# Optimization experiments

Measured on AMD Instinct MI355X. Metric: run time of the kernel, lower is better.

## Reference

```python
import jax, jax.numpy as jnp
import numpy as np

B, S, D = 4, 2048, 768
H = 12
HD = D // H  # 64


def setup_inputs() -> dict:
    key = jax.random.key(0)
    k1, k2, k3 = jax.random.split(key, 3)
    x = jax.random.normal(k1, (B, S, D), dtype=jnp.float32)
    w_qkv = jax.random.normal(k2, (D, 3 * D), dtype=jnp.float32) * (1.0 / np.sqrt(D))
    b_qkv = jnp.zeros((3 * D,), dtype=jnp.float32)
    w_proj = jax.random.normal(k3, (D, D), dtype=jnp.float32) * (1.0 / np.sqrt(D))
    b_proj = jnp.zeros((D,), dtype=jnp.float32)
    return {"x": x, "w_qkv": w_qkv, "b_qkv": b_qkv, "w_proj": w_proj, "b_proj": b_proj}


def reference(x, w_qkv, b_qkv, w_proj, b_proj):
    b, s, d = x.shape
    qkv = x @ w_qkv + b_qkv                      # [B,S,3D]
    q, k, v = jnp.split(qkv, 3, axis=-1)
    # [B,S,D] -> [B,H,S,HD]
    q = q.reshape(b, s, H, HD).transpose(0, 2, 1, 3)
    k = k.reshape(b, s, H, HD).transpose(0, 2, 1, 3)
    v = v.reshape(b, s, H, HD).transpose(0, 2, 1, 3)
    scores = jnp.einsum("bhqd,bhkd->bhqk", q, k) / jnp.sqrt(jnp.float32(HD))
    causal = jnp.tril(jnp.ones((s, s), dtype=bool))
    scores = jnp.where(causal[None, None, :, :], scores, jnp.float32(-jnp.inf))
    attn = jax.nn.softmax(scores, axis=-1)       # dropout p=0.0 -> identity
    out = jnp.einsum("bhqk,bhkd->bhqd", attn, v)  # [B,H,S,HD]
    out = out.transpose(0, 2, 1, 3).reshape(b, s, d)
    return out @ w_proj + b_proj
```

## Files before the change

### kernel.cpp

```cpp
#include <hip/hip_runtime.h>
#include <hip/hip_bf16.h>

typedef __hip_bfloat16 bf16;
typedef __bf16 bf16x8 __attribute__((ext_vector_type(8)));
typedef float f32x4 __attribute__((ext_vector_type(4)));

#define MFMA(a, b, c) __builtin_amdgcn_mfma_f32_16x16x32_bf16(a, b, c, 0, 0, 0)
#define EXP2F(x) __builtin_exp2f(x)

constexpr int Bn = 4, Sn = 2048, Dn = 768, Hn = 12;
constexpr int N3 = 3 * Dn;
constexpr int Mrows = Bn * Sn;

constexpr size_t XB_OFF    = 0;
constexpr size_t WQKV_OFF  = 12582912;
constexpr size_t WPROJ_OFF = 16121856;
constexpr size_t Q_OFF     = 17301504;
constexpr size_t K_OFF     = 29884416;
constexpr size_t VT_OFF    = 42467328;
constexpr size_t O_OFF     = 55050240;

#define QSCALE 0.1803368801111243f

__device__ __forceinline__ void gload16(const void* g, void* l) {
  __builtin_amdgcn_global_load_lds((__attribute__((address_space(1))) void*)g,
                                   (__attribute__((address_space(3))) void*)l,
                                   16, 0, 0);
}

__device__ __forceinline__ unsigned short f2bfu(float f) {
  __hip_bfloat16 h = __float2bfloat16(f);
  return *reinterpret_cast<unsigned short*>(&h);
}

__global__ __launch_bounds__(256) void cvt_x_kernel(const float* __restrict__ in,
                                                    bf16* __restrict__ out, int n4) {
  int i = blockIdx.x * 256 + threadIdx.x;
  if (i >= n4) return;
  float4 f = reinterpret_cast<const float4*>(in)[i];
  ushort4 o;
  o.x = f2bfu(f.x); o.y = f2bfu(f.y); o.z = f2bfu(f.z); o.w = f2bfu(f.w);
  reinterpret_cast<ushort4*>(out)[i] = o;
}

__global__ __launch_bounds__(256) void transpose_cvt(const float* __restrict__ in,
                                                     bf16* __restrict__ out, int K, int N) {
  __shared__ float tile[32][33];
  int n0 = blockIdx.x * 32, k0 = blockIdx.y * 32;
  int tx = threadIdx.x & 31, ty = threadIdx.x >> 5;
  for (int r = ty; r < 32; r += 8)
    tile[r][tx] = in[(size_t)(k0 + r) * N + n0 + tx];
  __syncthreads();
  for (int r = ty; r < 32; r += 8)
    out[(size_t)(n0 + r) * K + k0 + tx] = __float2bfloat16(tile[tx][r]);
}

__global__ __launch_bounds__(256) void gemm_qkv(const bf16* __restrict__ A,
                                                const bf16* __restrict__ BT,
                                                const float* __restrict__ bias,
                                                bf16* __restrict__ Qo,
                                                bf16* __restrict__ Ko,
                                                bf16* __restrict__ Vt) {
  __shared__ __align__(16) bf16 As[2][128 * 32];
  __shared__ __align__(16) bf16 Bs[2][128 * 32];
  const int tid = threadIdx.x;
  const int m0 = blockIdx.x * 128, n0 = blockIdx.y * 128;
  const int w = tid >> 6, lane = tid & 63;
  const int wr = w >> 1, wc = w & 1;
  const int lr = lane & 15, lg = lane >> 4;

  f32x4 acc[4][4] = {};

  auto stage = [&](int k0, int sb) {
    for (int r = 0; r < 2; ++r) {
      int c = tid + r * 256;
      int row = c >> 2, ch = c & 3;
      int gch = ch ^ ((row >> 1) & 3);
      gload16(A + (size_t)(m0 + row) * Dn + k0 + gch * 8, &As[sb][c * 8]);
      gload16(BT + (size_t)(n0 + row) * Dn + k0 + gch * 8, &Bs[sb][c * 8]);
    }
  };

  stage(0, 0);
  __syncthreads();

  const int sw = (lr >> 1) & 3;
  const int aoff = (wr * 64 + lr) * 32 + ((lg ^ sw) << 3);
  const int boff = (wc * 64 + lr) * 32 + ((lg ^ sw) << 3);
  int buf = 0;

  for (int kt = 0; kt < 24; ++kt) {
    if (kt < 23) stage((kt + 1) * 32, buf ^ 1);
    bf16x8 af[4], bfr[4];
    for (int mi = 0; mi < 4; ++mi)
      af[mi] = *reinterpret_cast<const bf16x8*>(&As[buf][aoff + mi * 512]);
    for (int ni = 0; ni < 4; ++ni)
      bfr[ni] = *reinterpret_cast<const bf16x8*>(&Bs[buf][boff + ni * 512]);
    for (int mi = 0; mi < 4; ++mi)
      for (int ni = 0; ni < 4; ++ni)
        acc[mi][ni] = MFMA(af[mi], bfr[ni], acc[mi][ni]);
    __syncthreads();
    buf ^= 1;
  }

  for (int ni = 0; ni < 4; ++ni) {
    const int col = n0 + wc * 64 + ni * 16 + lr;
    const float bv = bias[col];
    const int seg = (col >= Dn) + (col >= 2 * Dn);
    const int d = col - seg * Dn;
    const int h = d >> 6, hd = d & 63;
    for (int mi = 0; mi < 4; ++mi) {
      f32x4 v = acc[mi][ni];
      for (int r = 0; r < 4; ++r) {
        const int row = m0 + wr * 64 + mi * 16 + lg * 4 + r;
        const int b = row >> 11, s = row & 2047;
        const float val = v[r] + bv;
        const size_t bh = (size_t)(b * Hn + h);
        if (seg == 0)      Qo[(bh * Sn + s) * 64 + hd] = __float2bfloat16(val * QSCALE);
        else if (seg == 1) Ko[(bh * Sn + s) * 64 + hd] = __float2bfloat16(val);
        else               Vt[(bh * 64 + hd) * Sn + s] = __float2bfloat16(val);
      }
    }
  }
}

__global__ __launch_bounds__(256) void attn_fwd(const bf16* __restrict__ Q,
                                                const bf16* __restrict__ K,
                                                const bf16* __restrict__ Vt,
                                                bf16* __restrict__ O) {
  __shared__ __align__(16) bf16 Ks[2][64 * 64];
  __shared__ __align__(16) bf16 Vs[2][64 * 64];
  __shared__ __align__(16) bf16 Ps[4][16 * 64];
  const int tid = threadIdx.x, w = tid >> 6, lane = tid & 63;
  const int lr = lane & 15, lg = lane >> 4;
  const int bid = blockIdx.x;
  const int qt = 31 - (bid / 48);
  const int bh = bid % 48;
  const int q0 = qt * 64;
  const size_t base = (size_t)bh * Sn * 64;
  const int wrow = q0 + w * 16;

  bf16x8 qf[2];
  for (int kk = 0; kk < 2; ++kk)
    qf[kk] = *reinterpret_cast<const bf16x8*>(
        Q + base + (size_t)(wrow + lr) * 64 + kk * 32 + lg * 8);

  f32x4 o[4] = {};
  float mrow = -1e30f, lrow = 0.f;

  const int nt = qt + 1;

  auto stage = [&](int t, int sb) {
    for (int rr = 0; rr < 2; ++rr) {
      int c = tid + rr * 256;
      int row = c >> 3, cp = c & 7;
      int sc = cp ^ (row & 7);
      gload16(K + base + (size_t)t * 4096 + row * 64 + sc * 8, &Ks[sb][c * 8]);
      gload16(Vt + base + (size_t)row * Sn + t * 64 + sc * 8, &Vs[sb][c * 8]);
    }
  };

  stage(0, 0);
  __syncthreads();
  int buf = 0;
  for (int t = 0; t < nt; ++t) {
    if (t + 1 < nt) stage(t + 1, buf ^ 1);

    f32x4 sf[4];
    for (int ni = 0; ni < 4; ++ni) {
      const int krow = ni * 16 + lr;
      bf16x8 kf0 = *reinterpret_cast<const bf16x8*>(&Ks[buf][krow * 64 + (lg ^ (lr & 7)) * 8]);
      bf16x8 kf1 = *reinterpret_cast<const bf16x8*>(&Ks[buf][krow * 64 + ((4 + lg) ^ (lr & 7)) * 8]);
      f32x4 z = {};
      z = MFMA(kf0, qf[0], z);
      z = MFMA(kf1, qf[1], z);
      sf[ni] = z;
    }
    if (t == nt - 1) {
      const int qg = wrow + lr;
      for (int ni = 0; ni < 4; ++ni)
        for (int r = 0; r < 4; ++r) {
          int kg = t * 64 + ni * 16 + lg * 4 + r;
          if (kg > qg) sf[ni][r] = -1e30f;
        }
    }
    float ma = fmaxf(fmaxf(sf[0][0], sf[0][1]), fmaxf(sf[0][2], sf[0][3]));
    float mb = fmaxf(fmaxf(sf[1][0], sf[1][1]), fmaxf(sf[1][2], sf[1][3]));
    float mc = fmaxf(fmaxf(sf[2][0], sf[2][1]), fmaxf(sf[2][2], sf[2][3]));
    float md = fmaxf(fmaxf(sf[3][0], sf[3][1]), fmaxf(sf[3][2], sf[3][3]));
    float vmax = fmaxf(fmaxf(ma, mb), fmaxf(mc, md));
    vmax = fmaxf(vmax, __shfl_xor(vmax, 16));
    vmax = fmaxf(vmax, __shfl_xor(vmax, 32));
    const float mnew = fmaxf(mrow, vmax);
    const float alpha = EXP2F(mrow - mnew);
    float ps = 0.f;
    for (int ni = 0; ni < 4; ++ni) {
      f32x4 z = sf[ni];
      z[0] = EXP2F(z[0] - mnew);
      z[1] = EXP2F(z[1] - mnew);
      z[2] = EXP2F(z[2] - mnew);
      z[3] = EXP2F(z[3] - mnew);
      sf[ni] = z;
      ps += (z[0] + z[1]) + (z[2] + z[3]);
    }
    ps += __shfl_xor(ps, 16);
    ps += __shfl_xor(ps, 32);
    lrow = lrow * alpha + ps;
    mrow = mnew;
    for (int di = 0; di < 4; ++di) {
      f32x4 ov = o[di];
      ov[0] *= alpha; ov[1] *= alpha; ov[2] *= alpha; ov[3] *= alpha;
      o[di] = ov;
    }
    for (int ni = 0; ni < 4; ++ni) {
      const int chunk = ni * 2 + (lg >> 1);
      const int eoff = lr * 64 + ((chunk ^ (lr & 7)) << 3) + ((lg & 1) << 2);
      ushort4 pk;
      pk.x = f2bfu(sf[ni][0]); pk.y = f2bfu(sf[ni][1]);
      pk.z = f2bfu(sf[ni][2]); pk.w = f2bfu(sf[ni][3]);
      *reinterpret_cast<ushort4*>(&Ps[w][eoff]) = pk;
    }
    asm volatile("s_waitcnt lgkmcnt(0)" ::: "memory");
    __builtin_amdgcn_sched_barrier(0);
    for (int kk = 0; kk < 2; ++kk) {
      bf16x8 pf = *reinterpret_cast<const bf16x8*>(
          &Ps[w][lr * 64 + (((kk * 4 + lg) ^ (lr & 7)) << 3)]);
      for (int di = 0; di < 4; ++di) {
        bf16x8 vf = *reinterpret_cast<const bf16x8*>(
            &Vs[buf][(di * 16 + lr) * 64 + (((kk * 4 + lg) ^ (lr & 7)) << 3)]);
        o[di] = MFMA(vf, pf, o[di]);
      }
    }
    __syncthreads();
    buf ^= 1;
  }

  const int b = bh / Hn, h = bh % Hn;
  const float inv = 1.0f / lrow;
  const size_t rowbase = ((size_t)b * Sn + wrow + lr) * Dn + h * 64;
  for (int di = 0; di < 4; ++di) {
    f32x4 ov = o[di];
    ushort4 pk;
    pk.x = f2bfu(ov[0] * inv); pk.y = f2bfu(ov[1] * inv);
    pk.z = f2bfu(ov[2] * inv); pk.w = f2bfu(ov[3] * inv);
    *reinterpret_cast<ushort4*>(&O[rowbase + di * 16 + lg * 4]) = pk;
  }
}

__global__ __launch_bounds__(256) void gemm_proj(const bf16* __restrict__ A,
                                                 const bf16* __restrict__ BT,
                                                 const float* __restrict__ bias,
                                                 float* __restrict__ out) {
  __shared__ __align__(16) bf16 As[2][128 * 32];
  __shared__ __align__(16) bf16 Bs[2][128 * 32];
  const int tid = threadIdx.x;
  const int m0 = blockIdx.x * 128, n0 = blockIdx.y * 128;
  const int w = tid >> 6, lane = tid & 63;
  const int wr = w >> 1, wc = w & 1;
  const int lr = lane & 15, lg = lane >> 4;

  f32x4 acc[4][4] = {};

  auto stage = [&](int k0, int sb) {
    for (int r = 0; r < 2; ++r) {
      int c = tid + r * 256;
      int row = c >> 2, ch = c & 3;
      int gch = ch ^ ((row >> 1) & 3);
      gload16(A + (size_t)(m0 + row) * Dn + k0 + gch * 8, &As[sb][c * 8]);
      gload16(BT + (size_t)(n0 + row) * Dn + k0 + gch * 8, &Bs[sb][c * 8]);
    }
  };

  stage(0, 0);
  __syncthreads();

  const int sw = (lr >> 1) & 3;
  const int aoff = (wr * 64 + lr) * 32 + ((lg ^ sw) << 3);
  const int boff = (wc * 64 + lr) * 32 + ((lg ^ sw) << 3);
  int buf = 0;

  for (int kt = 0; kt < 24; ++kt) {
    if (kt < 23) stage((kt + 1) * 32, buf ^ 1);
    bf16x8 af[4], bfr[4];
    for (int mi = 0; mi < 4; ++mi)
      af[mi] = *reinterpret_cast<const bf16x8*>(&As[buf][aoff + mi * 512]);
    for (int ni = 0; ni < 4; ++ni)
      bfr[ni] = *reinterpret_cast<const bf16x8*>(&Bs[buf][boff + ni * 512]);
    for (int mi = 0; mi < 4; ++mi)
      for (int ni = 0; ni < 4; ++ni)
        acc[mi][ni] = MFMA(af[mi], bfr[ni], acc[mi][ni]);
    __syncthreads();
    buf ^= 1;
  }

  for (int ni = 0; ni < 4; ++ni) {
    const int col = n0 + wc * 64 + ni * 16 + lr;
    const float bv = bias[col];
    for (int mi = 0; mi < 4; ++mi) {
      f32x4 v = acc[mi][ni];
      for (int r = 0; r < 4; ++r) {
        const int row = m0 + wr * 64 + mi * 16 + lg * 4 + r;
        out[(size_t)row * Dn + col] = v[r] + bv;
      }
    }
  }
}

extern "C" void kernel_launch(void* const* d_in, const int* in_sizes, int n_in,
                              void* d_out, int out_size, void* d_ws, size_t ws_size,
                              hipStream_t stream) {
  const float* x      = (const float*)d_in[0];
  const float* w_qkv  = (const float*)d_in[1];
  const float* b_qkv  = (const float*)d_in[2];
  const float* w_proj = (const float*)d_in[3];
  const float* b_proj = (const float*)d_in[4];
  float* out = (float*)d_out;

  char* ws = (char*)d_ws;
  bf16* xb     = (bf16*)(ws + XB_OFF);
  bf16* wqkvT  = (bf16*)(ws + WQKV_OFF);
  bf16* wprojT = (bf16*)(ws + WPROJ_OFF);
  bf16* Qb     = (bf16*)(ws + Q_OFF);
  bf16* Kb     = (bf16*)(ws + K_OFF);
  bf16* Vtb    = (bf16*)(ws + VT_OFF);
  bf16* Ob     = (bf16*)(ws + O_OFF);

  cvt_x_kernel<<<(Mrows * Dn / 4 + 255) / 256, 256, 0, stream>>>(x, xb, Mrows * Dn / 4);
  transpose_cvt<<<dim3(N3 / 32, Dn / 32), 256, 0, stream>>>(w_qkv, wqkvT, Dn, N3);
  transpose_cvt<<<dim3(Dn / 32, Dn / 32), 256, 0, stream>>>(w_proj, wprojT, Dn, Dn);
  gemm_qkv<<<dim3(Mrows / 128, N3 / 128), 256, 0, stream>>>(xb, wqkvT, b_qkv, Qb, Kb, Vtb);
  attn_fwd<<<32 * 48, 256, 0, stream>>>(Qb, Kb, Vtb, Ob);
  gemm_proj<<<dim3(Mrows / 128, Dn / 128), 256, 0, stream>>>(Ob, wprojT, b_proj, out);
}
```

Before: 165.3 us.

## Use packed bf16 conversion, vectorize V stores, and skip lazy softmax rescale

Replaces scalar float-to-bf16 conversions with the packed v_cvt_pk_bf16_f32 instruction across the conversion, attention, and QKV epilogue paths. The V-transpose epilogue now writes four contiguous sequence elements in one 8-byte store instead of four scalar stores. The attention loop adds a lazy rescale: the running max and the O/l rescaling are updated only when some lane's new max exceeds the old one by more than a threshold. This saves exp and multiply work per tile, at the cost of allowing unnormalized exponentials up to 2^8, which slightly raises overflow and precision risk in bf16 P values.

```diff
diff --git a/kernel.cpp b/kernel.cpp
--- a/kernel.cpp
+++ b/kernel.cpp
@@ -28,9 +28,13 @@
                                    16, 0, 0);
 }
 
+__device__ __forceinline__ unsigned int cvt_pk_bf16(float lo, float hi) {
+  unsigned int r;
+  asm("v_cvt_pk_bf16_f32 %0, %1, %2" : "=v"(r) : "v"(lo), "v"(hi));
+  return r;
+}
 __device__ __forceinline__ unsigned short f2bfu(float f) {
-  __hip_bfloat16 h = __float2bfloat16(f);
-  return *reinterpret_cast<unsigned short*>(&h);
+  return (unsigned short)(cvt_pk_bf16(f, f) & 0xffffu);
 }
 
 __global__ __launch_bounds__(256) void cvt_x_kernel(const float* __restrict__ in,
@@ -38,9 +42,10 @@
   int i = blockIdx.x * 256 + threadIdx.x;
   if (i >= n4) return;
   float4 f = reinterpret_cast<const float4*>(in)[i];
-  ushort4 o;
-  o.x = f2bfu(f.x); o.y = f2bfu(f.y); o.z = f2bfu(f.z); o.w = f2bfu(f.w);
-  reinterpret_cast<ushort4*>(out)[i] = o;
+  uint2 o;
+  o.x = cvt_pk_bf16(f.x, f.y);
+  o.y = cvt_pk_bf16(f.z, f.w);
+  reinterpret_cast<uint2*>(out)[i] = o;
 }
 
 __global__ __launch_bounds__(256) void transpose_cvt(const float* __restrict__ in,
@@ -111,14 +116,20 @@
     const int h = d >> 6, hd = d & 63;
     for (int mi = 0; mi < 4; ++mi) {
       f32x4 v = acc[mi][ni];
-      for (int r = 0; r < 4; ++r) {
-        const int row = m0 + wr * 64 + mi * 16 + lg * 4 + r;
-        const int b = row >> 11, s = row & 2047;
-        const float val = v[r] + bv;
-        const size_t bh = (size_t)(b * Hn + h);
-        if (seg == 0)      Qo[(bh * Sn + s) * 64 + hd] = __float2bfloat16(val * QSCALE);
-        else if (seg == 1) Ko[(bh * Sn + s) * 64 + hd] = __float2bfloat16(val);
-        else               Vt[(bh * 64 + hd) * Sn + s] = __float2bfloat16(val);
+      const int row0 = m0 + wr * 64 + mi * 16 + lg * 4;
+      const int b = row0 >> 11, s0 = row0 & 2047;
+      const size_t bh = (size_t)(b * Hn + h);
+      if (seg == 2) {
+        uint2 pk;
+        pk.x = cvt_pk_bf16(v[0] + bv, v[1] + bv);
+        pk.y = cvt_pk_bf16(v[2] + bv, v[3] + bv);
+        *reinterpret_cast<uint2*>(&Vt[(bh * 64 + hd) * Sn + s0]) = pk;
+      } else if (seg == 0) {
+        for (int r = 0; r < 4; ++r)
+          Qo[(bh * Sn + s0 + r) * 64 + hd] = __float2bfloat16((v[r] + bv) * QSCALE);
+      } else {
+        for (int r = 0; r < 4; ++r)
+          Ko[(bh * Sn + s0 + r) * 64 + hd] = __float2bfloat16(v[r] + bv);
       }
     }
   }
@@ -191,34 +202,37 @@
     float vmax = fmaxf(fmaxf(ma, mb), fmaxf(mc, md));
     vmax = fmaxf(vmax, __shfl_xor(vmax, 16));
     vmax = fmaxf(vmax, __shfl_xor(vmax, 32));
-    const float mnew = fmaxf(mrow, vmax);
-    const float alpha = EXP2F(mrow - mnew);
+    if (!__all(vmax - mrow <= 8.0f)) {
+      const float mnew = fmaxf(mrow, vmax);
+      const float alpha = EXP2F(mrow - mnew);
+      lrow *= alpha;
+      for (int di = 0; di < 4; ++di) {
+        f32x4 ov = o[di];
+        ov[0] *= alpha; ov[1] *= alpha; ov[2] *= alpha; ov[3] *= alpha;
+        o[di] = ov;
+      }
+      mrow = mnew;
+    }
     float ps = 0.f;
     for (int ni = 0; ni < 4; ++ni) {
       f32x4 z = sf[ni];
-      z[0] = EXP2F(z[0] - mnew);
-      z[1] = EXP2F(z[1] - mnew);
-      z[2] = EXP2F(z[2] - mnew);
-      z[3] = EXP2F(z[3] - mnew);
+      z[0] = EXP2F(z[0] - mrow);
+      z[1] = EXP2F(z[1] - mrow);
+      z[2] = EXP2F(z[2] - mrow);
+      z[3] = EXP2F(z[3] - mrow);
       sf[ni] = z;
       ps += (z[0] + z[1]) + (z[2] + z[3]);
     }
     ps += __shfl_xor(ps, 16);
     ps += __shfl_xor(ps, 32);
-    lrow = lrow * alpha + ps;
-    mrow = mnew;
-    for (int di = 0; di < 4; ++di) {
-      f32x4 ov = o[di];
-      ov[0] *= alpha; ov[1] *= alpha; ov[2] *= alpha; ov[3] *= alpha;
-      o[di] = ov;
-    }
+    lrow += ps;
     for (int ni = 0; ni < 4; ++ni) {
       const int chunk = ni * 2 + (lg >> 1);
       const int eoff = lr * 64 + ((chunk ^ (lr & 7)) << 3) + ((lg & 1) << 2);
-      ushort4 pk;
-      pk.x = f2bfu(sf[ni][0]); pk.y = f2bfu(sf[ni][1]);
-      pk.z = f2bfu(sf[ni][2]); pk.w = f2bfu(sf[ni][3]);
-      *reinterpret_cast<ushort4*>(&Ps[w][eoff]) = pk;
+      uint2 pk;
+      pk.x = cvt_pk_bf16(sf[ni][0], sf[ni][1]);
+      pk.y = cvt_pk_bf16(sf[ni][2], sf[ni][3]);
+      *reinterpret_cast<uint2*>(&Ps[w][eoff]) = pk;
     }
     asm volatile("s_waitcnt lgkmcnt(0)" ::: "memory");
     __builtin_amdgcn_sched_barrier(0);
@@ -240,10 +254,10 @@
   const size_t rowbase = ((size_t)b * Sn + wrow + lr) * Dn + h * 64;
   for (int di = 0; di < 4; ++di) {
     f32x4 ov = o[di];
-    ushort4 pk;
-    pk.x = f2bfu(ov[0] * inv); pk.y = f2bfu(ov[1] * inv);
-    pk.z = f2bfu(ov[2] * inv); pk.w = f2bfu(ov[3] * inv);
-    *reinterpret_cast<ushort4*>(&O[rowbase + di * 16 + lg * 4]) = pk;
+    uint2 pk;
+    pk.x = cvt_pk_bf16(ov[0] * inv, ov[1] * inv);
+    pk.y = cvt_pk_bf16(ov[2] * inv, ov[3] * inv);
+    *reinterpret_cast<uint2*>(&O[rowbase + di * 16 + lg * 4]) = pk;
   }
 }
 
```

Measured after the change: 153.8 us. -7.0%, faster.
